# Optimization experiments

Measured on AMD Instinct MI355X. Metric: run time of the kernel, lower is better.

Reference implementation:

```python
import jax, jax.numpy as jnp
import numpy as np

B, N, D_MODEL = 4, 4096, 1024
N_HEADS, D_HEAD = 16, 64
NB_FEATURES = int(D_HEAD * np.log(D_HEAD))  # 266, performer default
EPS = 1e-4


def _gaussian_orthogonal_matrix(key, m, d):
    """performer-pytorch gaussian_orthogonal_random_matrix, scaling=0."""
    n_blocks = int(np.ceil(m / d))
    keys = jax.random.split(key, n_blocks + 1)
    blocks = []
    for i in range(n_blocks):
        g = jax.random.normal(keys[i], (d, d), jnp.float32)
        q, _ = jnp.linalg.qr(g)
        blocks.append(q.T)
    mat = jnp.concatenate(blocks, axis=0)[:m]  # [m, d]
    multiplier = jnp.linalg.norm(
        jax.random.normal(keys[-1], (m, d), jnp.float32), axis=1)
    return mat * multiplier[:, None]


def setup_inputs() -> dict:
    key = jax.random.key(0)
    ks = jax.random.split(key, 7)
    s = 1.0 / np.sqrt(D_MODEL)
    x = jax.random.normal(ks[0], (B, N, D_MODEL), jnp.float32)
    Wq = jax.random.normal(ks[1], (D_MODEL, D_MODEL), jnp.float32) * s
    Wk = jax.random.normal(ks[2], (D_MODEL, D_MODEL), jnp.float32) * s
    Wv = jax.random.normal(ks[3], (D_MODEL, D_MODEL), jnp.float32) * s
    Wo = jax.random.normal(ks[4], (D_MODEL, D_MODEL), jnp.float32) * s
    bo = jnp.zeros((D_MODEL,), jnp.float32)
    proj = _gaussian_orthogonal_matrix(ks[5], NB_FEATURES, D_HEAD)
    return {"x": x, "Wq": Wq, "Wk": Wk, "Wv": Wv, "Wo": Wo, "bo": bo,
            "proj": proj}


def _softmax_kernel(data, proj, is_query):
    # data: [b, h, n, d]; proj: [m, d]  (FAVOR+ positive random features)
    ratio = proj.shape[0] ** -0.5
    dn = data.shape[-1] ** -0.25  # data_normalizer
    dash = jnp.einsum('bhnd,md->bhnm', data * dn, proj)
    diag = 0.5 * (dn ** 2) * jnp.sum(data * data, axis=-1, keepdims=True)
    if is_query:
        stab = jnp.max(dash, axis=-1, keepdims=True)
    else:
        stab = jnp.max(dash, axis=(-2, -1), keepdims=True)
    return ratio * (jnp.exp(dash - diag - stab) + EPS)


def reference(x, Wq, Wk, Wv, Wo, bo, proj):
    b, n, _ = x.shape

    def split_heads(t):  # [b,n,D] -> [b,h,n,d]
        return t.reshape(b, n, N_HEADS, D_HEAD).transpose(0, 2, 1, 3)

    q = split_heads(x @ Wq)
    k = split_heads(x @ Wk)
    v = split_heads(x @ Wv)

    qp = _softmax_kernel(q, proj, True)   # [b,h,n,m]
    kp = _softmax_kernel(k, proj, False)  # [b,h,n,m]

    # non-causal linear attention
    k_sum = jnp.sum(kp, axis=2)                                # [b,h,m]
    d_inv = 1.0 / jnp.einsum('bhnm,bhm->bhn', qp, k_sum)       # [b,h,n]
    context = jnp.einsum('bhnm,bhnd->bhmd', kp, v)             # [b,h,m,d]
    out = jnp.einsum('bhnm,bhmd,bhn->bhnd', qp, context, d_inv)

    out = out.transpose(0, 2, 1, 3).reshape(b, n, N_HEADS * D_HEAD)
    return out @ Wo + bo
```

## Files before the change

kernel.cpp:

```cpp
#include <hip/hip_runtime.h>
#include <hip/hip_bf16.h>

typedef unsigned short u16;
typedef unsigned int   u32;
typedef __bf16 bf16x8 __attribute__((ext_vector_type(8)));
typedef float  f32x4  __attribute__((ext_vector_type(4)));
typedef unsigned short u16x8 __attribute__((ext_vector_type(8)));

#define B_    4
#define N_    4096
#define BN_   16384
#define DM_   1024
#define H_    16
#define BH_   64
#define M_    266
#define MP_   288
#define DN_    0.35355339059327373f
#define RATIO_ 0.061313933948496574f
#define EPS_   1e-4f

static __device__ __forceinline__ float b2f(u16 u) {
    union { u32 u; float f; } x; x.u = ((u32)u) << 16; return x.f;
}
static __device__ __forceinline__ u16 f2b(float f) {
    union { float f; u32 u; } x; x.f = f;
    u32 r = x.u + 0x7FFFu + ((x.u >> 16) & 1u);
    return (u16)(r >> 16);
}
static __device__ __forceinline__ u32 ford(float f) {
    u32 u = __float_as_uint(f);
    return (u & 0x80000000u) ? ~u : (u | 0x80000000u);
}
static __device__ __forceinline__ float forddec(u32 u) {
    return (u & 0x80000000u) ? __uint_as_float(u & 0x7FFFFFFFu) : __uint_as_float(~u);
}
static __device__ __forceinline__ f32x4 mfma16(bf16x8 a, bf16x8 b, f32x4 c) {
    return __builtin_amdgcn_mfma_f32_16x16x32_bf16(a, b, c, 0, 0, 0);
}
#define GLOAD16(gp, lp) __builtin_amdgcn_global_load_lds( \
    (const __attribute__((address_space(1))) void*)(gp),  \
    (__attribute__((address_space(3))) void*)(lp), 16, 0, 0)

__global__ __launch_bounds__(256) void pack_all(const float* __restrict__ x, u16* __restrict__ xb,
                                                const float* __restrict__ Wq, const float* __restrict__ Wk,
                                                const float* __restrict__ Wv, const float* __restrict__ Wo,
                                                u16* __restrict__ wT,
                                                const float* __restrict__ proj, u16* __restrict__ projb,
                                                u32* __restrict__ stabk) {
    __shared__ float tile[64][65];
    int bid = blockIdx.x, tid = threadIdx.x;
    if (bid < 16384) {
        int i = (bid * 256 + tid) * 4;
        float4 f = *reinterpret_cast<const float4*>(x + i);
        ushort4 o;
        o.x = f2b(f.x); o.y = f2b(f.y); o.z = f2b(f.z); o.w = f2b(f.w);
        *reinterpret_cast<ushort4*>(xb + i) = o;
    } else if (bid < 16384 + 1024) {
        int u = bid - 16384;
        int i0 = (u & 15) * 64;
        int j0 = (u >> 4) * 64;
        const float* src = (j0 < 1024) ? Wq : (j0 < 2048) ? Wk : (j0 < 3072) ? Wv : Wo;
        int jc = j0 & 1023;
        int tr = tid >> 6, tc = tid & 63;
#pragma unroll
        for (int it = 0; it < 16; ++it) {
            int r = it * 4 + tr;
            tile[r][tc] = src[(size_t)(i0 + r) * 1024 + jc + tc];
        }
        __syncthreads();
#pragma unroll
        for (int it = 0; it < 16; ++it) {
            int r = it * 4 + tr;
            wT[(size_t)(j0 + r) * 1024 + i0 + tc] = f2b(tile[tc][r]);
        }
    } else {
        int i = (bid - 17408) * 256 + tid;
        if (i < MP_ * 64) {
            int m = i >> 6;
            projb[i] = (m < M_) ? f2b(proj[i] * DN_) : (u16)0;
        }
        if (i < BH_) stabk[i] = 0u;
    }
}

template<int OUTF32>
__global__ __launch_bounds__(512, 1) void gemm256(const u16* __restrict__ A, const u16* __restrict__ Bt,
                                                  void* __restrict__ C, const float* __restrict__ bias,
                                                  int Ncols, int nby) {
    __shared__ u16 As[2][256 * 64];
    __shared__ u16 Bs[2][256 * 64];
    constexpr int K = 1024, T = 16;
    int tid = threadIdx.x, lane = tid & 63, wid = tid >> 6;
    int wm = wid >> 2, wn = wid & 3;
    int lr = lane & 15, lk8 = (lane >> 4) * 8;
    int nwg = gridDim.x;
    int wg = ((int)blockIdx.x & 7) * (nwg >> 3) + (int)blockIdx.x / 8;
    int u = wg % (8 * nby), pid = wg / (8 * nby);
    size_t r0 = (size_t)(pid * 8 + (u & 7)) * 256;
    size_t c0 = (size_t)(u / 8) * 256;

    auto stage = [&](int t, int h) {
        int buf = t & 1;
        const u16* src = (h < 2) ? (A + r0 * K) : (Bt + c0 * K);
        u16* dst = (h < 2) ? As[buf] : Bs[buf];
        int rbase = (h & 1) * 128;
        int kt = t * 64;
#pragma unroll
        for (int c = 0; c < 2; ++c) {
            int li0 = rbase * 8 + c * 512 + wid * 64;
            int li = li0 + lane;
            int row = li >> 3, kk = (li & 7) * 8;
            int kks = kk ^ ((row & 7) << 3);
            GLOAD16(&src[(size_t)row * K + kt + kks], (char*)dst + (size_t)li0 * 16);
        }
    };
    auto lda = [&](int buf, int mf, int ks) {
        int row = wm * 128 + mf * 16 + lr;
        return *reinterpret_cast<const bf16x8*>(&As[buf][row * 64 + ((ks * 32 + lk8) ^ ((row & 7) << 3))]);
    };
    auto ldb = [&](int buf, int nf, int ks) {
        int row = wn * 64 + nf * 16 + lr;
        return *reinterpret_cast<const bf16x8*>(&Bs[buf][row * 64 + ((ks * 32 + lk8) ^ ((row & 7) << 3))]);
    };

    f32x4 acc[8][4] = {};
    stage(0, 0); stage(0, 1); stage(0, 2); stage(0, 3);
    stage(1, 2); stage(1, 3); stage(1, 0);
    asm volatile("s_waitcnt vmcnt(6)" ::: "memory");
    __builtin_amdgcn_s_barrier();

#pragma unroll 2
    for (int t = 0; t < T; ++t) {
        const int buf = t & 1;
        bf16x8 av[4][2], aw[4][2], bv[4][2];
#pragma unroll
        for (int mf = 0; mf < 4; ++mf) { av[mf][0] = lda(buf, mf, 0); av[mf][1] = lda(buf, mf, 1); }
#pragma unroll
        for (int nf = 0; nf < 4; ++nf) { bv[nf][0] = ldb(buf, nf, 0); bv[nf][1] = ldb(buf, nf, 1); }
        if (t + 1 < T) stage(t + 1, 1);
        __builtin_amdgcn_s_barrier();
        __builtin_amdgcn_s_setprio(1);
#pragma unroll
        for (int mf = 0; mf < 4; ++mf)
#pragma unroll
            for (int nf = 0; nf < 4; ++nf) {
                acc[mf][nf] = mfma16(av[mf][0], bv[nf][0], acc[mf][nf]);
                acc[mf][nf] = mfma16(av[mf][1], bv[nf][1], acc[mf][nf]);
            }
        __builtin_amdgcn_s_setprio(0);
        __builtin_amdgcn_s_barrier();
#pragma unroll
        for (int mf = 0; mf < 4; ++mf) { aw[mf][0] = lda(buf, 4 + mf, 0); aw[mf][1] = lda(buf, 4 + mf, 1); }
        if (t + 2 < T) stage(t + 2, 2);
        __builtin_amdgcn_s_barrier();
        __builtin_amdgcn_s_setprio(1);
#pragma unroll
        for (int mf = 0; mf < 4; ++mf)
#pragma unroll
            for (int nf = 0; nf < 2; ++nf) {
                acc[4 + mf][nf] = mfma16(aw[mf][0], bv[nf][0], acc[4 + mf][nf]);
                acc[4 + mf][nf] = mfma16(aw[mf][1], bv[nf][1], acc[4 + mf][nf]);
            }
        __builtin_amdgcn_s_setprio(0);
        __builtin_amdgcn_s_barrier();
        if (t + 2 < T) { stage(t + 2, 3); stage(t + 2, 0); }
        __builtin_amdgcn_s_barrier();
        __builtin_amdgcn_s_setprio(1);
#pragma unroll
        for (int mf = 0; mf < 4; ++mf)
#pragma unroll
            for (int nf = 0; nf < 2; ++nf) {
                acc[4 + mf][2 + nf] = mfma16(aw[mf][0], bv[2 + nf][0], acc[4 + mf][2 + nf]);
                acc[4 + mf][2 + nf] = mfma16(aw[mf][1], bv[2 + nf][1], acc[4 + mf][2 + nf]);
            }
        __builtin_amdgcn_s_setprio(0);
        if (t + 2 < T) asm volatile("s_waitcnt vmcnt(6)" ::: "memory");
        else           asm volatile("s_waitcnt vmcnt(0)" ::: "memory");
        __builtin_amdgcn_s_barrier();
    }

    int rq = (lane >> 4) * 4;
#pragma unroll
    for (int mf = 0; mf < 8; ++mf)
#pragma unroll
        for (int nf = 0; nf < 4; ++nf) {
            size_t col = c0 + wn * 64 + nf * 16 + lr;
#pragma unroll
            for (int r = 0; r < 4; ++r) {
                size_t row = r0 + wm * 128 + mf * 16 + rq + r;
                float v = acc[mf][nf][r];
                if (OUTF32) reinterpret_cast<float*>(C)[row * Ncols + col] = v + bias[col];
                else        reinterpret_cast<u16*>(C)[row * Ncols + col] = f2b(v);
            }
        }
}

__global__ __launch_bounds__(256) void dashk_max(const u16* __restrict__ qkv, const u16* __restrict__ projb,
                                                 u32* __restrict__ stabk) {
    __shared__ u16 kt[128 * 64];
    __shared__ float redbuf[4];
    int bh = blockIdx.y, ch = blockIdx.x;
    int b = bh >> 4, h = bh & 15;
    const u16* src = qkv + ((size_t)(b * N_ + ch * 128)) * 3072 + 1024 + h * 64;
    int tid = threadIdx.x;
#pragma unroll
    for (int c = 0; c < 4; ++c) {
        int li = c * 256 + tid;
        int row = li >> 3, kk = (li & 7) * 8;
        *reinterpret_cast<bf16x8*>(&kt[row * 64 + (kk ^ ((row & 7) << 3))]) =
            *reinterpret_cast<const bf16x8*>(&src[(size_t)row * 3072 + kk]);
    }
    __syncthreads();
    int lane = tid & 63, wid = tid >> 6;
    int lr = lane & 15, lk8 = (lane >> 4) * 8;
    float mx = -3.0e38f;
#pragma unroll
    for (int i = 0; i < 2; ++i) {
        int row = wid * 32 + i * 16 + lr;
        bf16x8 a0 = *reinterpret_cast<const bf16x8*>(&kt[row * 64 + (lk8 ^ ((row & 7) << 3))]);
        bf16x8 a1 = *reinterpret_cast<const bf16x8*>(&kt[row * 64 + ((32 + lk8) ^ ((row & 7) << 3))]);
#pragma unroll
        for (int mf = 0; mf < 17; ++mf) {
            f32x4 d = {0.f, 0.f, 0.f, 0.f};
            const u16* pb = projb + (size_t)(mf * 16 + lr) * 64;
            d = mfma16(a0, *reinterpret_cast<const bf16x8*>(pb + lk8), d);
            d = mfma16(a1, *reinterpret_cast<const bf16x8*>(pb + 32 + lk8), d);
            if (mf * 16 + lr < M_)
                mx = fmaxf(mx, fmaxf(fmaxf(d[0], d[1]), fmaxf(d[2], d[3])));
        }
    }
#pragma unroll
    for (int off = 32; off >= 1; off >>= 1) mx = fmaxf(mx, __shfl_xor(mx, off, 64));
    if (lane == 0) redbuf[wid] = mx;
    __syncthreads();
    if (tid == 0) {
        float m = fmaxf(fmaxf(redbuf[0], redbuf[1]), fmaxf(redbuf[2], redbuf[3]));
        atomicMax(&stabk[bh], ford(m));
    }
}

__global__ __launch_bounds__(512, 2) void kp_context(const u16* __restrict__ qkv, const u16* __restrict__ projb,
                                                     const u32* __restrict__ stabk,
                                                     float* __restrict__ ctx_part, float* __restrict__ ksum_part) {
    __shared__ u16 kt[2][64 * 64];
    __shared__ u16 vt[2][64 * 64];
    __shared__ u16 kpT[MP_ * 64];
    __shared__ float ksum_s[4][MP_];
    int bh = blockIdx.y, ch = blockIdx.x;
    int b = bh >> 4, h = bh & 15;
    int tid = threadIdx.x, lane = tid & 63, wid = tid >> 6;
    int grp = wid >> 2, wid4 = wid & 3;
    int lr = lane & 15, lk8 = (lane >> 4) * 8, rq = (lane >> 4) * 4;
    float stab = forddec(stabk[bh]);
    float ksump[9];
#pragma unroll
    for (int i = 0; i < 9; ++i) ksump[i] = 0.f;
    f32x4 acc[9] = {};
    int drow = wid4 * 16 + lr;

    auto stage_kv = [&](int sc, int buf) {
        int n0 = ch * 512 + sc * 64;
        const u16* srck = qkv + ((size_t)(b * N_ + n0)) * 3072 + 1024 + h * 64;
        const u16* srcv = srck + 1024;
        int li0 = wid * 64;
        int li = li0 + lane;
        int row = li >> 3, kk = (li & 7) * 8;
        int kks = kk ^ ((row & 7) << 3);
        GLOAD16(&srck[(size_t)row * 3072 + kks], (char*)kt[buf] + (size_t)li0 * 16);
        GLOAD16(&srcv[(size_t)row * 3072 + kks], (char*)vt[buf] + (size_t)li0 * 16);
    };

    stage_kv(0, 0);
    asm volatile("s_waitcnt vmcnt(0)" ::: "memory");
    for (int sc = 0; sc < 8; ++sc) {
        int buf = sc & 1;
        __builtin_amdgcn_s_barrier();
        if (sc < 7) stage_kv(sc + 1, buf ^ 1);
        {
            int row = wid4 * 16 + lr;
            bf16x8 a0 = *reinterpret_cast<const bf16x8*>(&kt[buf][row * 64 + (lk8 ^ ((row & 7) << 3))]);
            bf16x8 a1 = *reinterpret_cast<const bf16x8*>(&kt[buf][row * 64 + ((32 + lk8) ^ ((row & 7) << 3))]);
            float ss = 0.f;
#pragma unroll
            for (int j = 0; j < 8; ++j) {
                float f0 = (float)a0[j]; ss = fmaf(f0, f0, ss);
                float f1 = (float)a1[j]; ss = fmaf(f1, f1, ss);
            }
            ss += __shfl_xor(ss, 16, 64);
            ss += __shfl_xor(ss, 32, 64);
            float dgk[4];
#pragma unroll
            for (int r = 0; r < 4; ++r) dgk[r] = 0.0625f * __shfl(ss, rq + r, 64);
            int c4 = wid4 * 16 + rq;
#pragma unroll
            for (int mf = 0; mf < 9; ++mf) {
                int mfg = grp * 9 + mf;
                f32x4 d = {0.f, 0.f, 0.f, 0.f};
                const u16* pb = projb + (size_t)(mfg * 16 + lr) * 64;
                d = mfma16(a0, *reinterpret_cast<const bf16x8*>(pb + lk8), d);
                d = mfma16(a1, *reinterpret_cast<const bf16x8*>(pb + 32 + lk8), d);
                int m = mfg * 16 + lr;
                bool real = (m < M_);
                ushort4 o;
                float v0 = real ? RATIO_ * (__expf(d[0] - dgk[0] - stab) + EPS_) : 0.f;
                float v1 = real ? RATIO_ * (__expf(d[1] - dgk[1] - stab) + EPS_) : 0.f;
                float v2 = real ? RATIO_ * (__expf(d[2] - dgk[2] - stab) + EPS_) : 0.f;
                float v3 = real ? RATIO_ * (__expf(d[3] - dgk[3] - stab) + EPS_) : 0.f;
                o.x = f2b(v0); o.y = f2b(v1); o.z = f2b(v2); o.w = f2b(v3);
                ksump[mf] += v0 + v1 + v2 + v3;
                *reinterpret_cast<ushort4*>(&kpT[m * 64 + (c4 ^ ((m & 7) << 3))]) = o;
            }
        }
        asm volatile("s_waitcnt lgkmcnt(0)" ::: "memory");
        __builtin_amdgcn_s_barrier();
        bf16x8 bv[2];
#pragma unroll
        for (int ks = 0; ks < 2; ++ks) {
            union { u16 s[8]; bf16x8 v; } tmp;
#pragma unroll
            for (int j = 0; j < 8; ++j) {
                int n = ks * 32 + lk8 + j;
                tmp.s[j] = vt[buf][n * 64 + ((drow & ~7) ^ ((n & 7) << 3)) + (drow & 7)];
            }
            bv[ks] = tmp.v;
        }
#pragma unroll
        for (int ks = 0; ks < 2; ++ks) {
#pragma unroll
            for (int mf = 0; mf < 9; ++mf) {
                int mrow = (grp * 9 + mf) * 16 + lr;
                bf16x8 av = *reinterpret_cast<const bf16x8*>(
                    &kpT[mrow * 64 + ((ks * 32 + lk8) ^ ((mrow & 7) << 3))]);
                acc[mf] = mfma16(av, bv[ks], acc[mf]);
            }
        }
        if (sc < 7) asm volatile("s_waitcnt vmcnt(0)" ::: "memory");
    }
    size_t basep = ((size_t)ch * BH_ + bh) * MP_;
#pragma unroll
    for (int mf = 0; mf < 9; ++mf) {
#pragma unroll
        for (int r = 0; r < 4; ++r) {
            int m = (grp * 9 + mf) * 16 + rq + r;
            ctx_part[(basep + m) * 64 + wid4 * 16 + lr] = acc[mf][r];
        }
    }
#pragma unroll
    for (int mf = 0; mf < 9; ++mf) {
        float v = ksump[mf];
        v += __shfl_xor(v, 16, 64);
        v += __shfl_xor(v, 32, 64);
        if (lane < 16) ksum_s[wid4][(grp * 9 + mf) * 16 + lane] = v;
    }
    __syncthreads();
    for (int t = tid; t < MP_; t += 512)
        ksum_part[basep + t] = ksum_s[0][t] + ksum_s[1][t] + ksum_s[2][t] + ksum_s[3][t];
}

__global__ __launch_bounds__(256) void reduce_all(const float* __restrict__ ctx_part,
                                                  const float* __restrict__ ksum_part,
                                                  u16* __restrict__ ctx2, float* __restrict__ ksum) {
    int bid = blockIdx.x, tid = threadIdx.x;
    if (bid < 576) {
        int t = bid * 256 + tid;
        int mo = t % 36;
        int rest = t / 36;
        int d = rest & 63;
        int bh = rest >> 6;
        u16x8 o;
#pragma unroll
        for (int mm = 0; mm < 8; ++mm) {
            int m = mo * 8 + mm;
            float s = 0.f;
#pragma unroll
            for (int c = 0; c < 8; ++c)
                s += ctx_part[(((size_t)c * BH_ + bh) * MP_ + m) * 64 + d];
            o[mm] = f2b(s);
        }
        size_t idx = ((((size_t)bh * 4 + (d >> 4)) * 9 + (mo >> 2)) * 64
                      + (mo & 3) * 16 + (d & 15)) * 8;
        *reinterpret_cast<u16x8*>(ctx2 + idx) = o;
    } else {
        int t = (bid - 576) * 256 + tid;
        float s = 0.f;
#pragma unroll
        for (int c = 0; c < 8; ++c) s += ksum_part[(size_t)c * BH_ * MP_ + t];
        ksum[t] = s;
    }
}

__global__ __launch_bounds__(256) void qp_out(const u16* __restrict__ qkv, const u16* __restrict__ projb,
                                              const float* __restrict__ ksum,
                                              const u16* __restrict__ ctx2, u16* __restrict__ attn) {
    __shared__ u16 qt[64 * 64];
    __shared__ u16 qp_s[64 * 296];
    int bh = blockIdx.y, ch = blockIdx.x;
    int b = bh >> 4, h = bh & 15;
    int tid = threadIdx.x, lane = tid & 63, wid = tid >> 6;
    int lr = lane & 15, lk8 = (lane >> 4) * 8, rq = (lane >> 4) * 4;
    float ksh[18];
#pragma unroll
    for (int mf = 0; mf < 18; ++mf) ksh[mf] = ksum[bh * MP_ + mf * 16 + lr];
    const u16* srcq = qkv + ((size_t)(b * N_ + ch * 128)) * 3072 + h * 64;
    int srow = tid >> 2, skk = (tid & 3) * 16;
    int ssw = (srow & 7) << 3;
    int sd0 = srow * 64 + (skk ^ ssw);
    int sd1 = srow * 64 + ((skk + 8) ^ ssw);
    {
        u16x8 qa = *reinterpret_cast<const u16x8*>(&srcq[(size_t)srow * 3072 + skk]);
        u16x8 qb = *reinterpret_cast<const u16x8*>(&srcq[(size_t)srow * 3072 + skk + 8]);
        *reinterpret_cast<u16x8*>(&qt[sd0]) = qa;
        *reinterpret_cast<u16x8*>(&qt[sd1]) = qb;
    }
    asm volatile("s_waitcnt lgkmcnt(0)" ::: "memory");
    __builtin_amdgcn_s_barrier();
#pragma unroll
    for (int c = 0; c < 2; ++c) {
        int n0 = ch * 128 + c * 64;
        int row = wid * 16 + lr;
        bf16x8 a0 = *reinterpret_cast<const bf16x8*>(&qt[row * 64 + (lk8 ^ ((row & 7) << 3))]);
        bf16x8 a1 = *reinterpret_cast<const bf16x8*>(&qt[row * 64 + ((32 + lk8) ^ ((row & 7) << 3))]);
        u16x8 qa, qb;
        if (c == 0) {
            qa = *reinterpret_cast<const u16x8*>(&srcq[(size_t)(64 + srow) * 3072 + skk]);
            qb = *reinterpret_cast<const u16x8*>(&srcq[(size_t)(64 + srow) * 3072 + skk + 8]);
        }
        float ss = 0.f;
#pragma unroll
        for (int j = 0; j < 8; ++j) {
            float f0 = (float)a0[j]; ss = fmaf(f0, f0, ss);
            float f1 = (float)a1[j]; ss = fmaf(f1, f1, ss);
        }
        ss += __shfl_xor(ss, 16, 64);
        ss += __shfl_xor(ss, 32, 64);
        float dq[4];
#pragma unroll
        for (int r = 0; r < 4; ++r) dq[r] = 0.0625f * __shfl(ss, rq + r, 64);
        f32x4 dall[18];
        float mx[4] = {-3e38f, -3e38f, -3e38f, -3e38f};
#pragma unroll
        for (int mf = 0; mf < 18; ++mf) {
            f32x4 d = {0.f, 0.f, 0.f, 0.f};
            const u16* pb = projb + (size_t)(mf * 16 + lr) * 64;
            d = mfma16(a0, *reinterpret_cast<const bf16x8*>(pb + lk8), d);
            d = mfma16(a1, *reinterpret_cast<const bf16x8*>(pb + 32 + lk8), d);
            dall[mf] = d;
            if (mf * 16 + lr < M_) {
#pragma unroll
                for (int r = 0; r < 4; ++r) mx[r] = fmaxf(mx[r], d[r]);
            }
        }
#pragma unroll
        for (int r = 0; r < 4; ++r) {
#pragma unroll
            for (int off = 1; off < 16; off <<= 1)
                mx[r] = fmaxf(mx[r], __shfl_xor(mx[r], off, 64));
        }
        float den[4] = {0.f, 0.f, 0.f, 0.f};
#pragma unroll
        for (int mf = 0; mf < 18; ++mf) {
            int m = mf * 16 + lr;
            bool real = (m < M_);
#pragma unroll
            for (int r = 0; r < 4; ++r) {
                float qv = real ? RATIO_ * (__expf(dall[mf][r] - dq[r] - mx[r]) + EPS_) : 0.f;
                qp_s[(wid * 16 + rq + r) * 296 + m] = f2b(qv);
                den[r] = fmaf(qv, ksh[mf], den[r]);
            }
        }
        float dinv[4];
#pragma unroll
        for (int r = 0; r < 4; ++r) {
            float s = den[r];
#pragma unroll
            for (int off = 1; off < 16; off <<= 1) s += __shfl_xor(s, off, 64);
            dinv[r] = 1.0f / s;
        }
        __builtin_amdgcn_s_barrier();
        if (c == 0) {
            *reinterpret_cast<u16x8*>(&qt[sd0]) = qa;
            *reinterpret_cast<u16x8*>(&qt[sd1]) = qb;
        }
        bf16x8 aq[9];
#pragma unroll
        for (int ks = 0; ks < 9; ++ks)
            aq[ks] = *reinterpret_cast<const bf16x8*>(&qp_s[(wid * 16 + lr) * 296 + ks * 32 + lk8]);
#pragma unroll
        for (int df = 0; df < 4; ++df) {
            f32x4 o = {0.f, 0.f, 0.f, 0.f};
            const u16* pb = ctx2 + ((((size_t)bh * 4 + df) * 9) * 64 + lane) * 8;
#pragma unroll
            for (int ks = 0; ks < 9; ++ks)
                o = mfma16(aq[ks], *reinterpret_cast<const bf16x8*>(pb + (size_t)ks * 512), o);
#pragma unroll
            for (int r = 0; r < 4; ++r) {
                size_t orow = (size_t)b * N_ + n0 + wid * 16 + rq + r;
                attn[orow * 1024 + h * 64 + df * 16 + lr] = f2b(o[r] * dinv[r]);
            }
        }
        if (c == 0) {
            asm volatile("s_waitcnt lgkmcnt(0)" ::: "memory");
            __builtin_amdgcn_s_barrier();
        }
    }
}

extern "C" void kernel_launch(void* const* d_in, const int* in_sizes, int n_in,
                              void* d_out, int out_size, void* d_ws, size_t ws_size,
                              hipStream_t stream) {
    const float* x    = (const float*)d_in[0];
    const float* Wq   = (const float*)d_in[1];
    const float* Wk   = (const float*)d_in[2];
    const float* Wv   = (const float*)d_in[3];
    const float* Wo   = (const float*)d_in[4];
    const float* bo   = (const float*)d_in[5];
    const float* proj = (const float*)d_in[6];
    char* ws = (char*)d_ws;
    u16*   xb    = (u16*)(ws + 0);
    u16*   wT    = (u16*)(ws + 33554432);
    u16*   qkv   = (u16*)(ws + 41943040);
    u16*   projb = (u16*)(ws + 142606336);
    u32*   stabk = (u32*)(ws + 144740352);
    float* ksum  = (float*)(ws + 144740608);
    u16*   ctx2  = (u16*)(ws + 144814336);
    float* ctxp  = (float*)(ws + 147173632);
    float* ksump = (float*)(ws + 184922368);
    u16*   attn  = (u16*)(ws + 185512192);
    float* out   = (float*)d_out;

    pack_all<<<17480, 256, 0, stream>>>(x, xb, Wq, Wk, Wv, Wo, wT, proj, projb, stabk);
    gemm256<0><<<768, 512, 0, stream>>>(xb, wT, (void*)qkv, nullptr, 3072, 12);
    dashk_max<<<dim3(32, 64), 256, 0, stream>>>(qkv, projb, stabk);
    kp_context<<<dim3(8, 64), 512, 0, stream>>>(qkv, projb, stabk, ctxp, ksump);
    reduce_all<<<648, 256, 0, stream>>>(ctxp, ksump, ctx2, ksum);
    qp_out<<<dim3(32, 64), 256, 0, stream>>>(qkv, projb, ksum, ctx2, attn);
    gemm256<1><<<256, 512, 0, stream>>>(attn, wT + 3072 * 1024, (void*)out, bo, 1024, 4);
}
```

Baseline: 407.1 us.

## Stage bf16 GEMM epilogue through LDS and use nontemporal loads/stores

The bf16 GEMM epilogue now writes its accumulator tile into the reused shared memory with an XOR swizzle, then emits coalesced 16-byte stores instead of scattered 2-byte stores. Nontemporal load/store builtins are also applied across pack, reduce, context and output kernels to bypass cache retention for streaming data. Nontemporal hints could hurt where a later kernel rereads the data from L2/MALL, such as qkv or ctx_part. The shared-memory staging adds a barrier.

```diff
diff --git a/kernel.cpp b/kernel.cpp
--- a/kernel.cpp
+++ b/kernel.cpp
@@ -5,7 +5,9 @@
 typedef unsigned int   u32;
 typedef __bf16 bf16x8 __attribute__((ext_vector_type(8)));
 typedef float  f32x4  __attribute__((ext_vector_type(4)));
+typedef float  f32x4v __attribute__((ext_vector_type(4)));
 typedef unsigned short u16x8 __attribute__((ext_vector_type(8)));
+typedef unsigned short u16x4 __attribute__((ext_vector_type(4)));
 
 #define B_    4
 #define N_    4096
@@ -40,6 +42,8 @@
 #define GLOAD16(gp, lp) __builtin_amdgcn_global_load_lds( \
     (const __attribute__((address_space(1))) void*)(gp),  \
     (__attribute__((address_space(3))) void*)(lp), 16, 0, 0)
+#define NTST(v, p) __builtin_nontemporal_store((v), (p))
+#define NTLD(p)    __builtin_nontemporal_load((p))
 
 __global__ __launch_bounds__(256) void pack_all(const float* __restrict__ x, u16* __restrict__ xb,
                                                 const float* __restrict__ Wq, const float* __restrict__ Wk,
@@ -51,10 +55,10 @@
     int bid = blockIdx.x, tid = threadIdx.x;
     if (bid < 16384) {
         int i = (bid * 256 + tid) * 4;
-        float4 f = *reinterpret_cast<const float4*>(x + i);
-        ushort4 o;
-        o.x = f2b(f.x); o.y = f2b(f.y); o.z = f2b(f.z); o.w = f2b(f.w);
-        *reinterpret_cast<ushort4*>(xb + i) = o;
+        f32x4v f = NTLD(reinterpret_cast<const f32x4v*>(x + i));
+        u16x4 o;
+        o[0] = f2b(f[0]); o[1] = f2b(f[1]); o[2] = f2b(f[2]); o[3] = f2b(f[3]);
+        NTST(o, reinterpret_cast<u16x4*>(xb + i));
     } else if (bid < 16384 + 1024) {
         int u = bid - 16384;
         int i0 = (u & 15) * 64;
@@ -65,13 +69,13 @@
 #pragma unroll
         for (int it = 0; it < 16; ++it) {
             int r = it * 4 + tr;
-            tile[r][tc] = src[(size_t)(i0 + r) * 1024 + jc + tc];
+            tile[r][tc] = NTLD(&src[(size_t)(i0 + r) * 1024 + jc + tc]);
         }
         __syncthreads();
 #pragma unroll
         for (int it = 0; it < 16; ++it) {
             int r = it * 4 + tr;
-            wT[(size_t)(j0 + r) * 1024 + i0 + tc] = f2b(tile[tc][r]);
+            NTST(f2b(tile[tc][r]), &wT[(size_t)(j0 + r) * 1024 + i0 + tc]);
         }
     } else {
         int i = (bid - 17408) * 256 + tid;
@@ -87,8 +91,7 @@
 __global__ __launch_bounds__(512, 1) void gemm256(const u16* __restrict__ A, const u16* __restrict__ Bt,
                                                   void* __restrict__ C, const float* __restrict__ bias,
                                                   int Ncols, int nby) {
-    __shared__ u16 As[2][256 * 64];
-    __shared__ u16 Bs[2][256 * 64];
+    __shared__ u16 sm[65536];
     constexpr int K = 1024, T = 16;
     int tid = threadIdx.x, lane = tid & 63, wid = tid >> 6;
     int wm = wid >> 2, wn = wid & 3;
@@ -102,7 +105,7 @@
     auto stage = [&](int t, int h) {
         int buf = t & 1;
         const u16* src = (h < 2) ? (A + r0 * K) : (Bt + c0 * K);
-        u16* dst = (h < 2) ? As[buf] : Bs[buf];
+        u16* dst = sm + ((h < 2) ? 0 : 32768) + buf * 16384;
         int rbase = (h & 1) * 128;
         int kt = t * 64;
 #pragma unroll
@@ -116,11 +119,13 @@
     };
     auto lda = [&](int buf, int mf, int ks) {
         int row = wm * 128 + mf * 16 + lr;
-        return *reinterpret_cast<const bf16x8*>(&As[buf][row * 64 + ((ks * 32 + lk8) ^ ((row & 7) << 3))]);
+        return *reinterpret_cast<const bf16x8*>(
+            &sm[buf * 16384 + row * 64 + ((ks * 32 + lk8) ^ ((row & 7) << 3))]);
     };
     auto ldb = [&](int buf, int nf, int ks) {
         int row = wn * 64 + nf * 16 + lr;
-        return *reinterpret_cast<const bf16x8*>(&Bs[buf][row * 64 + ((ks * 32 + lk8) ^ ((row & 7) << 3))]);
+        return *reinterpret_cast<const bf16x8*>(
+            &sm[32768 + buf * 16384 + row * 64 + ((ks * 32 + lk8) ^ ((row & 7) << 3))]);
     };
 
     f32x4 acc[8][4] = {};
@@ -180,19 +185,43 @@
     }
 
     int rq = (lane >> 4) * 4;
-#pragma unroll
-    for (int mf = 0; mf < 8; ++mf)
-#pragma unroll
-        for (int nf = 0; nf < 4; ++nf) {
-            size_t col = c0 + wn * 64 + nf * 16 + lr;
-#pragma unroll
-            for (int r = 0; r < 4; ++r) {
-                size_t row = r0 + wm * 128 + mf * 16 + rq + r;
-                float v = acc[mf][nf][r];
-                if (OUTF32) reinterpret_cast<float*>(C)[row * Ncols + col] = v + bias[col];
-                else        reinterpret_cast<u16*>(C)[row * Ncols + col] = f2b(v);
-            }
-        }
+    if (OUTF32) {
+#pragma unroll
+        for (int mf = 0; mf < 8; ++mf)
+#pragma unroll
+            for (int nf = 0; nf < 4; ++nf) {
+                size_t col = c0 + wn * 64 + nf * 16 + lr;
+                float bs = bias[col];
+#pragma unroll
+                for (int r = 0; r < 4; ++r) {
+                    size_t row = r0 + wm * 128 + mf * 16 + rq + r;
+                    NTST(acc[mf][nf][r] + bs, &reinterpret_cast<float*>(C)[row * Ncols + col]);
+                }
+            }
+    } else {
+#pragma unroll
+        for (int mf = 0; mf < 8; ++mf)
+#pragma unroll
+            for (int nf = 0; nf < 4; ++nf) {
+                int cb = (wn * 64 + nf * 16 + lr) * 2;
+#pragma unroll
+                for (int r = 0; r < 4; ++r) {
+                    int row = wm * 128 + mf * 16 + rq + r;
+                    *reinterpret_cast<u16*>((char*)sm + row * 512 + (cb ^ ((row & 15) << 4))) =
+                        f2b(acc[mf][nf][r]);
+                }
+            }
+        __syncthreads();
+        u16* Cu = reinterpret_cast<u16*>(C);
+#pragma unroll
+        for (int p = 0; p < 16; ++p) {
+            int li = p * 512 + tid;
+            int row = li >> 5, c8 = li & 31;
+            u16x8 v = *reinterpret_cast<const u16x8*>(
+                (char*)sm + row * 512 + ((c8 * 16) ^ ((row & 15) << 4)));
+            NTST(v, reinterpret_cast<u16x8*>(&Cu[(r0 + row) * (size_t)Ncols + c0 + c8 * 8]));
+        }
+    }
 }
 
 __global__ __launch_bounds__(256) void dashk_max(const u16* __restrict__ qkv, const u16* __restrict__ projb,
@@ -342,7 +371,7 @@
 #pragma unroll
         for (int r = 0; r < 4; ++r) {
             int m = (grp * 9 + mf) * 16 + rq + r;
-            ctx_part[(basep + m) * 64 + wid4 * 16 + lr] = acc[mf][r];
+            NTST(acc[mf][r], &ctx_part[(basep + m) * 64 + wid4 * 16 + lr]);
         }
     }
 #pragma unroll
@@ -354,7 +383,7 @@
     }
     __syncthreads();
     for (int t = tid; t < MP_; t += 512)
-        ksum_part[basep + t] = ksum_s[0][t] + ksum_s[1][t] + ksum_s[2][t] + ksum_s[3][t];
+        NTST(ksum_s[0][t] + ksum_s[1][t] + ksum_s[2][t] + ksum_s[3][t], &ksum_part[basep + t]);
 }
 
 __global__ __launch_bounds__(256) void reduce_all(const float* __restrict__ ctx_part,
@@ -374,18 +403,18 @@
             float s = 0.f;
 #pragma unroll
             for (int c = 0; c < 8; ++c)
-                s += ctx_part[(((size_t)c * BH_ + bh) * MP_ + m) * 64 + d];
+                s += NTLD(&ctx_part[(((size_t)c * BH_ + bh) * MP_ + m) * 64 + d]);
             o[mm] = f2b(s);
         }
         size_t idx = ((((size_t)bh * 4 + (d >> 4)) * 9 + (mo >> 2)) * 64
                       + (mo & 3) * 16 + (d & 15)) * 8;
-        *reinterpret_cast<u16x8*>(ctx2 + idx) = o;
+        NTST(o, reinterpret_cast<u16x8*>(ctx2 + idx));
     } else {
         int t = (bid - 576) * 256 + tid;
         float s = 0.f;
 #pragma unroll
-        for (int c = 0; c < 8; ++c) s += ksum_part[(size_t)c * BH_ * MP_ + t];
-        ksum[t] = s;
+        for (int c = 0; c < 8; ++c) s += NTLD(&ksum_part[(size_t)c * BH_ * MP_ + t]);
+        NTST(s, &ksum[t]);
     }
 }
 
@@ -495,7 +524,7 @@
 #pragma unroll
             for (int r = 0; r < 4; ++r) {
                 size_t orow = (size_t)b * N_ + n0 + wid * 16 + rq + r;
-                attn[orow * 1024 + h * 64 + df * 16 + lr] = f2b(o[r] * dinv[r]);
+                NTST(f2b(o[r] * dinv[r]), &attn[orow * 1024 + h * 64 + df * 16 + lr]);
             }
         }
         if (c == 0) {
```

Result: slower. 487.0 us (+19.6%).
